# Performance work log

Hardware: AMD Instinct MI355X
Metric: run time of the kernel (lower is better)

The kernel has to match this reference:

```python
import jax, jax.numpy as jnp
import numpy as np

N = 4096        # nodes
F_IN = 256      # in_features
F_OUT = 64      # out_features
H = 64          # lstm_out_features
MAX_DEG = 64    # max neighbor count == max packed seq length
ALPHA = 0.2     # leaky relu negative slope
NEG = -9e15


def setup_inputs() -> dict:
    key = jax.random.key(0)
    ks = jax.random.split(key, 8)
    h = jax.random.normal(ks[0], (N, F_IN), dtype=jnp.float32)
    # per-node neighbor counts in [1, MAX_DEG]
    seq_length = jax.random.randint(ks[1], (N,), 1, MAX_DEG + 1, dtype=jnp.int32)
    # adjacency with exactly seq_length[i] ones in row i
    r = jax.random.uniform(ks[2], (N, N))
    ranks = jnp.argsort(jnp.argsort(-r, axis=1), axis=1)
    adj = (ranks < seq_length[:, None]).astype(jnp.float32)
    # parameters (xavier-ish scale)
    W = jax.random.normal(ks[3], (F_IN, F_OUT), dtype=jnp.float32) * (2.0 / (F_IN + F_OUT)) ** 0.5
    a = jax.random.normal(ks[4], (2 * F_OUT, 1), dtype=jnp.float32) * 0.1
    # backward-direction LSTM weights (torch gate order i,f,g,o); forward dir is unused in output
    w_ih = jax.random.normal(ks[5], (4 * H, F_OUT), dtype=jnp.float32) * 0.1
    w_hh = jax.random.normal(ks[6], (4 * H, H), dtype=jnp.float32) * 0.1
    b_ih = jnp.zeros((4 * H,), dtype=jnp.float32)
    b_hh = jnp.zeros((4 * H,), dtype=jnp.float32)
    return {"h": h, "adj": adj, "seq_length": seq_length, "W": W, "a": a,
            "w_ih": w_ih, "w_hh": w_hh, "b_ih": b_ih, "b_hh": b_hh}


def reference(h, adj, seq_length, W, a, w_ih, w_hh, b_ih, b_hh):
    n = h.shape[0]
    Wh = h @ W                                   # [N, F_OUT]
    # e[i,j] = leakyrelu(a_left . Wh_i + a_right . Wh_j)  (same math as O(N^2) concat)
    a1, a2 = a[:F_OUT, 0], a[F_OUT:, 0]
    e = jax.nn.leaky_relu((Wh @ a1)[:, None] + (Wh @ a2)[None, :], negative_slope=ALPHA)
    att = jax.nn.softmax(jnp.where(adj > 0, e, NEG), axis=1)   # [N, N]
    Wh2 = att @ Wh                               # aggregated node features [N, F_OUT]
    # sort neighbors by descending attention; LSTM only reads the first seq_length[i] <= MAX_DEG
    order = jnp.argsort(-att, axis=1)[:, :MAX_DEG]            # [N, T]
    seq = Wh2[order]                              # [N, T, F_OUT]
    # backward LSTM direction == run forward over the length-reversed sequence
    t = jnp.arange(MAX_DEG)
    rev_idx = jnp.clip(seq_length[:, None] - 1 - t[None, :], 0)
    rev = jnp.take_along_axis(seq, rev_idx[:, :, None], axis=1)  # [N, T, F_OUT]
    mask = t[None, :] < seq_length[:, None]                       # [N, T]

    def cell(carry, xm):
        hs, cs = carry
        x, m = xm                                 # x: [N, F_OUT], m: [N]
        gates = x @ w_ih.T + hs @ w_hh.T + b_ih + b_hh
        i, f, g, o = jnp.split(gates, 4, axis=1)
        c_new = jax.nn.sigmoid(f) * cs + jax.nn.sigmoid(i) * jnp.tanh(g)
        h_new = jax.nn.sigmoid(o) * jnp.tanh(c_new)
        m = m[:, None]
        return (jnp.where(m, h_new, hs), jnp.where(m, c_new, cs)), None

    init = (jnp.zeros((n, H), Wh.dtype), jnp.zeros((n, H), Wh.dtype))
    xs = (jnp.swapaxes(rev, 0, 1), mask.T)        # time-major
    (hn, _), _ = jax.lax.scan(cell, init, xs)
    return hn                                     # [N, H]  == torch hn[-1] (backward dir)
```

## Files before the change

kernel.cpp:

```cpp
#include <hip/hip_runtime.h>
#include <hip/hip_bf16.h>
#include <math.h>

#define N_NODES 4096
#define F_INN   256
#define F_OUTT  64
#define HID     64
#define MAXDEG  64

typedef __attribute__((ext_vector_type(8))) short bf16x8;
typedef __attribute__((ext_vector_type(4))) float f32x4;

__device__ int    g_mode;
__device__ int    g_anyArr[64];
__device__ float  g_Wh [N_NODES * F_OUTT];
__device__ float  g_s1 [N_NODES];
__device__ float  g_s2 [N_NODES];
__device__ int    g_rev[N_NODES * MAXDEG];
__device__ int    g_perm[N_NODES];
__device__ int    g_nbr[N_NODES * MAXDEG];
__device__ int    g_cnt[N_NODES];
__device__ float  g_WihT[64 * 256];
__device__ float  g_bias[256];
__device__ float4 g_GX [N_NODES * F_OUTT];

__device__ __forceinline__ float bf2f(unsigned short u) {
  union { unsigned int i; float f; } v; v.i = ((unsigned int)u) << 16; return v.f;
}
__device__ __forceinline__ unsigned short f2bf(float f) {
  union { __hip_bfloat16 b; unsigned short u; } v; v.b = __float2bfloat16(f); return v.u;
}

__device__ __forceinline__ float bcastf(float v, int l) {
  return __int_as_float(__builtin_amdgcn_readlane(__float_as_int(v), l));
}

__device__ __forceinline__ float rcp_fast(float x) { return __builtin_amdgcn_rcpf(x); }

__device__ __forceinline__ float sigm(float x) {
  return rcp_fast(1.f + __expf(-x));
}
__device__ __forceinline__ float tanh_fast(float x) {
  return fmaf(-2.f, rcp_fast(1.f + __expf(2.f * x)), 1.f);
}

__device__ __forceinline__ int mbcnt64(unsigned long long m) {
  return __builtin_amdgcn_mbcnt_hi((unsigned)(m >> 32),
         __builtin_amdgcn_mbcnt_lo((unsigned)(m & 0xFFFFFFFFull), 0));
}

__device__ __forceinline__ bf16x8 zfrag() {
  bf16x8 z;
  #pragma unroll
  for (int i = 0; i < 8; i++) z[i] = 0;
  return z;
}

__device__ __forceinline__ void block_sync_lds() {
  __asm__ volatile("s_waitcnt lgkmcnt(0)" ::: "memory");
  __builtin_amdgcn_s_barrier();
}

#define MFMA16(a, b, c) __builtin_amdgcn_mfma_f32_16x16x32_bf16((a), (b), (c), 0, 0, 0)

__global__ __launch_bounds__(256) void k_detect(const unsigned int* __restrict__ aw) {
  __shared__ int any;
  if (threadIdx.x == 0) any = 0;
  __syncthreads();
  const uint4 v = ((const uint4*)aw)[blockIdx.x * 256 + threadIdx.x];
  int loc = (int)((v.x & 0xFFFFu) | (v.y & 0xFFFFu) | (v.z & 0xFFFFu) | (v.w & 0xFFFFu));
  if (loc) atomicOr(&any, 1);
  __syncthreads();
  if (threadIdx.x == 0) g_anyArr[blockIdx.x] = any;
}

__global__ __launch_bounds__(256) void k_sort(const int* __restrict__ seq) {
  __shared__ int hist[MAXDEG + 1];
  __shared__ int offs[MAXDEG + 1];
  const int tid = threadIdx.x;
  if (tid <= MAXDEG) hist[tid] = 0;
  __syncthreads();
  if (tid == 0) {
    int any = 0;
    for (int b = 0; b < 64; b++) any |= g_anyArr[b];
    g_mode = any ? 1 : 0;
  }
  for (int i = tid; i < N_NODES; i += 256)
    atomicAdd(&hist[min(max(seq[i], 0), MAXDEG)], 1);
  __syncthreads();
  if (tid == 0) {
    int run = 0;
    for (int L = MAXDEG; L >= 0; L--) { offs[L] = run; run += hist[L]; }
  }
  __syncthreads();
  for (int i = tid; i < N_NODES; i += 256) {
    int p = atomicAdd(&offs[min(max(seq[i], 0), MAXDEG)], 1);
    g_perm[p] = i;
  }
}

__global__ __launch_bounds__(256) void k_scan(
    const void* __restrict__ adj, const void* __restrict__ w_ih,
    const void* __restrict__ b_ih, const void* __restrict__ b_hh)
{
  const bool bf16 = (g_mode == 1);
  const int i = blockIdx.x;
  const int w = threadIdx.x >> 6, lane = threadIdx.x & 63;
  __shared__ int seg[4][MAXDEG];
  __shared__ int scnt[4];

  if (i < 64) {
    const int unit = threadIdx.x >> 2, g = threadIdx.x & 3;
    const int src = (g * 64 + unit) * F_OUTT + i;
    g_WihT[i * 256 + threadIdx.x] =
        bf16 ? bf2f(((const unsigned short*)w_ih)[src]) : ((const float*)w_ih)[src];
  } else if (i == 64) {
    const int t = threadIdx.x;
    g_bias[t] = bf16 ? (bf2f(((const unsigned short*)b_ih)[t]) +
                        bf2f(((const unsigned short*)b_hh)[t]))
                     : (((const float*)b_ih)[t] + ((const float*)b_hh)[t]);
  }

  int base = 0;
  if (bf16) {
    const uint4* ar = (const uint4*)((const unsigned short*)adj + (size_t)i * N_NODES);
    #pragma unroll
    for (int it = 0; it < 2; it++) {
      const uint4 v = ar[w * 128 + it * 64 + lane];
      unsigned word[4] = {v.x, v.y, v.z, v.w};
      bool nz[8];
      #pragma unroll
      for (int k = 0; k < 4; k++) {
        nz[2 * k]     = (word[k] & 0x0000FFFFu) != 0u;
        nz[2 * k + 1] = (word[k] & 0xFFFF0000u) != 0u;
      }
      int pre = 0, tot = 0;
      #pragma unroll
      for (int k = 0; k < 8; k++) {
        unsigned long long bl = __ballot(nz[k]);
        pre += mbcnt64(bl);
        tot += __popcll(bl);
      }
      int loc = 0;
      #pragma unroll
      for (int k = 0; k < 8; k++) {
        if (nz[k]) {
          int p = base + pre + loc;
          if (p < MAXDEG) seg[w][p] = w * 1024 + it * 512 + lane * 8 + k;
          loc++;
        }
      }
      base += tot;
    }
  } else {
    const float4* ar = (const float4*)((const float*)adj + (size_t)i * N_NODES);
    #pragma unroll
    for (int it = 0; it < 4; it++) {
      const float4 v = ar[w * 256 + it * 64 + lane];
      bool nz[4] = {v.x != 0.0f, v.y != 0.0f, v.z != 0.0f, v.w != 0.0f};
      int pre = 0, tot = 0;
      #pragma unroll
      for (int k = 0; k < 4; k++) {
        unsigned long long bl = __ballot(nz[k]);
        pre += mbcnt64(bl);
        tot += __popcll(bl);
      }
      int loc = 0;
      #pragma unroll
      for (int k = 0; k < 4; k++) {
        if (nz[k]) {
          int p = base + pre + loc;
          if (p < MAXDEG) seg[w][p] = w * 1024 + it * 256 + lane * 4 + k;
          loc++;
        }
      }
      base += tot;
    }
  }
  if (lane == 0) scnt[w] = base;
  __syncthreads();
  int off = 0;
  #pragma unroll
  for (int u = 0; u < 4; u++) off += (u < w) ? scnt[u] : 0;
  const int cw = min(scnt[w], MAXDEG);
  if (lane < cw) {
    const int p = off + lane;
    if (p < MAXDEG) g_nbr[i * MAXDEG + p] = seg[w][lane];
  }
  if (threadIdx.x == 0)
    g_cnt[i] = min(scnt[0] + scnt[1] + scnt[2] + scnt[3], MAXDEG);
}

__global__ __launch_bounds__(256) void k_wh(
    const void* __restrict__ h, const void* __restrict__ W, const void* __restrict__ a)
{
  const bool bf16 = (g_mode == 1);
  __shared__ float Ws[F_INN * F_OUTT];
  const int tid = threadIdx.x;
  if (bf16) {
    const ushort4* Wu = (const ushort4*)W;
    for (int v = tid; v < F_INN * F_OUTT / 4; v += 256) {
      ushort4 u = Wu[v];
      ((float4*)Ws)[v] = make_float4(bf2f(u.x), bf2f(u.y), bf2f(u.z), bf2f(u.w));
    }
  } else {
    const float4* Wf = (const float4*)W;
    for (int v = tid; v < F_INN * F_OUTT / 4; v += 256) ((float4*)Ws)[v] = Wf[v];
  }
  __syncthreads();
  const int wave = tid >> 6, lane = tid & 63;
  const int row0 = blockIdx.x * 16 + wave * 4;

  float hr[4][4];
  #pragma unroll
  for (int r = 0; r < 4; r++) {
    if (bf16) {
      ushort4 v = ((const ushort4*)((const unsigned short*)h + (row0 + r) * F_INN))[lane];
      hr[0][r] = bf2f(v.x); hr[1][r] = bf2f(v.y); hr[2][r] = bf2f(v.z); hr[3][r] = bf2f(v.w);
    } else {
      float4 v = ((const float4*)((const float*)h + (row0 + r) * F_INN))[lane];
      hr[0][r] = v.x; hr[1][r] = v.y; hr[2][r] = v.z; hr[3][r] = v.w;
    }
  }

  double acc[4] = {0.0, 0.0, 0.0, 0.0};
  #pragma unroll 4
  for (int l = 0; l < 64; l++) {
    #pragma unroll
    for (int j = 0; j < 4; j++) {
      const double wd = (double)Ws[(l * 4 + j) * F_OUTT + lane];
      #pragma unroll
      for (int r = 0; r < 4; r++)
        acc[r] += (double)bcastf(hr[j][r], l) * wd;
    }
  }

  float a1, a2;
  if (bf16) {
    a1 = bf2f(((const unsigned short*)a)[lane]);
    a2 = bf2f(((const unsigned short*)a)[F_OUTT + lane]);
  } else {
    a1 = ((const float*)a)[lane];
    a2 = ((const float*)a)[F_OUTT + lane];
  }

  #pragma unroll
  for (int r = 0; r < 4; r++) {
    const float whv = (float)acc[r];
    g_Wh[(row0 + r) * F_OUTT + lane] = whv;
    double t1 = (double)whv * (double)a1;
    double t2 = (double)whv * (double)a2;
    #pragma unroll
    for (int off = 32; off > 0; off >>= 1) {
      t1 += __shfl_down(t1, off);
      t2 += __shfl_down(t2, off);
    }
    if (lane == 0) { g_s1[row0 + r] = (float)t1; g_s2[row0 + r] = (float)t2; }
  }
}

__global__ __launch_bounds__(64) void k_att2(void) {
  const int lane = threadIdx.x & 63;
  const int i = blockIdx.x;

  __shared__ int srt[MAXDEG];

  const int L = __builtin_amdgcn_readfirstlane(min(g_cnt[i], MAXDEG));
  int jn = 0;
  if (lane < L) jn = g_nbr[i * MAXDEG + lane] & (N_NODES - 1);

  const float s2v = g_s2[jn];
  float av;
  {
    float s = g_s1[i] + s2v;
    float e = (s > 0.0f) ? s : 0.2f * s;
    if (lane >= L) e = -3.0e38f;
    float m = e;
    #pragma unroll
    for (int off = 32; off > 0; off >>= 1) m = fmaxf(m, __shfl_xor(m, off));
    float p = (lane < L) ? __expf(e - m) : 0.0f;
    float ssum = p;
    #pragma unroll
    for (int off = 32; off > 0; off >>= 1) ssum += __shfl_xor(ssum, off);
    av = p * rcp_fast(ssum);
    int rank = 0;
    for (int qq = 0; qq < L; qq++) {
      const float aq = bcastf(av, qq);
      const int   jq = __builtin_amdgcn_readlane(jn, qq);
      rank += (aq > av || (aq == av && jq < jn)) ? 1 : 0;
    }
    if (lane < L) srt[rank] = jn;
  }
  g_rev[i * MAXDEG + lane] = (lane < L) ? srt[L - 1 - lane] : 0;

  float a0 = 0.f, a1 = 0.f, a2 = 0.f, a3 = 0.f;
  float a4 = 0.f, a5 = 0.f, a6 = 0.f, a7 = 0.f;
  int q = 0;
  for (; q + 8 <= L; q += 8) {
    a0 = fmaf(bcastf(av, q    ), g_Wh[(size_t)__builtin_amdgcn_readlane(jn, q    ) * F_OUTT + lane], a0);
    a1 = fmaf(bcastf(av, q + 1), g_Wh[(size_t)__builtin_amdgcn_readlane(jn, q + 1) * F_OUTT + lane], a1);
    a2 = fmaf(bcastf(av, q + 2), g_Wh[(size_t)__builtin_amdgcn_readlane(jn, q + 2) * F_OUTT + lane], a2);
    a3 = fmaf(bcastf(av, q + 3), g_Wh[(size_t)__builtin_amdgcn_readlane(jn, q + 3) * F_OUTT + lane], a3);
    a4 = fmaf(bcastf(av, q + 4), g_Wh[(size_t)__builtin_amdgcn_readlane(jn, q + 4) * F_OUTT + lane], a4);
    a5 = fmaf(bcastf(av, q + 5), g_Wh[(size_t)__builtin_amdgcn_readlane(jn, q + 5) * F_OUTT + lane], a5);
    a6 = fmaf(bcastf(av, q + 6), g_Wh[(size_t)__builtin_amdgcn_readlane(jn, q + 6) * F_OUTT + lane], a6);
    a7 = fmaf(bcastf(av, q + 7), g_Wh[(size_t)__builtin_amdgcn_readlane(jn, q + 7) * F_OUTT + lane], a7);
  }
  for (; q < L; q++)
    a0 = fmaf(bcastf(av, q), g_Wh[(size_t)__builtin_amdgcn_readlane(jn, q) * F_OUTT + lane], a0);
  const float wh2v = ((a0 + a1) + (a2 + a3)) + ((a4 + a5) + (a6 + a7));

  float gx0 = 0.f, gx1 = 0.f, gx2 = 0.f, gx3 = 0.f;
  #pragma unroll
  for (int f = 0; f < 64; f++) {
    const float wf = bcastf(wh2v, f);
    const float4 cv = *(const float4*)(g_WihT + f * 256 + lane * 4);
    gx0 = fmaf(cv.x, wf, gx0);
    gx1 = fmaf(cv.y, wf, gx1);
    gx2 = fmaf(cv.z, wf, gx2);
    gx3 = fmaf(cv.w, wf, gx3);
  }
  gx0 += g_bias[0 * 64 + lane];
  gx1 += g_bias[1 * 64 + lane];
  gx2 += g_bias[2 * 64 + lane];
  gx3 += g_bias[3 * 64 + lane];
  g_GX[(size_t)i * F_OUTT + lane] = make_float4(gx0, gx1, gx2, gx3);
}

__global__ __launch_bounds__(256, 2) void k_lstm_mfma(
    const void* __restrict__ w_hh, const int* __restrict__ seq,
    void* __restrict__ out)
{
  const bool bf16 = (g_mode == 1);
  __shared__ __align__(16) unsigned short lds_h[2][16 * 72];
  __shared__ int lds_idx[8][MAXDEG];
  const int tid = threadIdx.x;
  const int w = tid >> 6, lane = tid & 63;
  const int q = lane >> 4, c = lane & 15;
  const int rb = blockIdx.x * 8;

  for (int v = tid; v < 2 * 16 * 72; v += 256) ((unsigned short*)lds_h)[v] = 0;

  for (int v = tid; v < 8 * MAXDEG; v += 256) {
    const int e = v >> 6, t0 = v & (MAXDEG - 1);
    const int row = g_perm[rb + e] & (N_NODES - 1);
    lds_idx[e][t0] = g_rev[row * MAXDEG + t0] & (N_NODES - 1);
  }

  const int Lmax = min(max(seq[g_perm[rb] & (N_NODES - 1)], 0), MAXDEG);

  int rows_c[4];
  #pragma unroll
  for (int r = 0; r < 4; r++) rows_c[r] = min(q * 4 + r, 7);

  int row_own[2], Ls_own[2];
  #pragma unroll
  for (int k = 0; k < 2; k++) {
    row_own[k] = g_perm[rb + 2 * q + k] & (N_NODES - 1);
    Ls_own[k]  = min(max(seq[row_own[k]], 0), MAXDEG);
  }
  const int d_unit = 16 * w + c;
  const int sl = ((lane >> 5) << 4) | c;
  const bool qodd = (q & 1) != 0;

  bf16x8 Bhi[4][2];
  #pragma unroll
  for (int g = 0; g < 4; g++) {
    const int col = 64 * g + d_unit;
    #pragma unroll
    for (int ch = 0; ch < 2; ch++) {
      if (bf16) {
        Bhi[g][ch] = *(const bf16x8*)((const unsigned short*)w_hh + (size_t)col * 64 + ch * 32 + q * 8);
      } else {
        const float* wp = (const float*)w_hh + (size_t)col * 64 + ch * 32 + q * 8;
        float4 va = *(const float4*)wp, vb = *(const float4*)(wp + 4);
        bf16x8 f;
        f[0] = (short)f2bf(va.x); f[1] = (short)f2bf(va.y);
        f[2] = (short)f2bf(va.z); f[3] = (short)f2bf(va.w);
        f[4] = (short)f2bf(vb.x); f[5] = (short)f2bf(vb.y);
        f[6] = (short)f2bf(vb.z); f[7] = (short)f2bf(vb.w);
        Bhi[g][ch] = f;
      }
    }
  }

  __syncthreads();

  float4 gxb[4][4];
  #pragma unroll
  for (int s = 0; s < 4; s++) {
    #pragma unroll
    for (int r = 0; r < 4; r++)
      gxb[s][r] = g_GX[lds_idx[rows_c[r]][s] * F_OUTT + d_unit];
  }
  int idx_cur[4];
  #pragma unroll
  for (int r = 0; r < 4; r++) idx_cur[r] = lds_idx[rows_c[r]][4];

  bf16x8 h0 = zfrag(), h1 = zfrag();
  float cst[2] = {0.f, 0.f}, hst[2] = {0.f, 0.f};
  const int Lr = (Lmax + 3) & ~3;

  for (int t = 0; t < Lr; t += 4) {
    #pragma unroll
    for (int j = 0; j < 4; j++) {
      const int tt = t + j;
      f32x4 acc[4];
      #pragma unroll
      for (int g = 0; g < 4; g++) {
        f32x4 a;
        a[0] = (g==0)?gxb[j][0].x:(g==1)?gxb[j][0].y:(g==2)?gxb[j][0].z:gxb[j][0].w;
        a[1] = (g==0)?gxb[j][1].x:(g==1)?gxb[j][1].y:(g==2)?gxb[j][1].z:gxb[j][1].w;
        a[2] = (g==0)?gxb[j][2].x:(g==1)?gxb[j][2].y:(g==2)?gxb[j][2].z:gxb[j][2].w;
        a[3] = (g==0)?gxb[j][3].x:(g==1)?gxb[j][3].y:(g==2)?gxb[j][3].z:gxb[j][3].w;
        a = MFMA16(h0, Bhi[g][0], a);
        a = MFMA16(h1, Bhi[g][1], a);
        acc[g] = a;
      }
      #pragma unroll
      for (int r = 0; r < 4; r++)
        gxb[j][r] = g_GX[idx_cur[r] * F_OUTT + d_unit];
      {
        const int nt = min(tt + 5, MAXDEG - 1);
        #pragma unroll
        for (int r = 0; r < 4; r++) idx_cur[r] = lds_idx[rows_c[r]][nt];
      }
      float gv[4][2];
      #pragma unroll
      for (int g = 0; g < 4; g++) {
        float t0v = __shfl(acc[g][0], sl);
        float t1v = __shfl(acc[g][1], sl);
        float t2v = __shfl(acc[g][2], sl);
        float t3v = __shfl(acc[g][3], sl);
        gv[g][0] = qodd ? t2v : t0v;
        gv[g][1] = qodd ? t3v : t1v;
      }
      unsigned short* lh = lds_h[j & 1];
      #pragma unroll
      for (int k = 0; k < 2; k++) {
        float ig = sigm(gv[0][k]);
        float fg = sigm(gv[1][k]);
        float gg = tanh_fast(gv[2][k]);
        float og = sigm(gv[3][k]);
        float cn = fg * cst[k] + ig * gg;
        float hn = og * tanh_fast(cn);
        bool live = (tt < Ls_own[k]);
        cst[k] = live ? cn : cst[k];
        hst[k] = live ? hn : hst[k];
        lh[(2 * q + k) * 72 + d_unit] = f2bf(hst[k]);
      }
      block_sync_lds();
      {
        const unsigned short* lr_ = lds_h[j & 1] + c * 72;
        h0 = *(const bf16x8*)(lr_ + 8 * q);
        h1 = *(const bf16x8*)(lr_ + 32 + 8 * q);
      }
    }
  }
  #pragma unroll
  for (int k = 0; k < 2; k++) {
    if (bf16) ((__hip_bfloat16*)out)[row_own[k] * HID + d_unit] = __float2bfloat16(hst[k]);
    else      ((float*)out)[row_own[k] * HID + d_unit] = hst[k];
  }
}

extern "C" void kernel_launch(void* const* d_in, const int* in_sizes, int n_in,
                              void* d_out, int out_size, void* d_ws, size_t ws_size,
                              hipStream_t stream) {
  (void)in_sizes; (void)n_in; (void)out_size; (void)d_ws; (void)ws_size;
  const void* h    = d_in[0];
  const void* adj  = d_in[1];
  const int*  seq  = (const int*)d_in[2];
  const void* W    = d_in[3];
  const void* a    = d_in[4];
  const void* w_ih = d_in[5];
  const void* w_hh = d_in[6];
  const void* b_ih = d_in[7];
  const void* b_hh = d_in[8];

  k_detect   <<<64,           256, 0, stream>>>((const unsigned int*)adj);
  k_sort     <<<1,            256, 0, stream>>>(seq);
  k_scan     <<<N_NODES,      256, 0, stream>>>(adj, w_ih, b_ih, b_hh);
  k_wh       <<<N_NODES / 16, 256, 0, stream>>>(h, W, a);
  k_att2     <<<N_NODES,      64,  0, stream>>>();
  k_lstm_mfma<<<N_NODES / 8,  256, 0, stream>>>(w_hh, seq, d_out);
}
```

Before: 200.0 us.

## Run LSTM recurrence in a single wavefront per block to drop barriers

Restructures the LSTM kernel from 4 wavefronts handling 8 rows to one 64-lane wavefront handling 4 rows, so each wave computes all 16 gate column tiles with MFMA and exchanges gate values through LDS instead of shuffles. This removes the per-timestep block barrier and double-buffered hidden state, since a single wave needs no cross-wave sync. In exchange each wave issues 4x more MFMAs per step (only 4 of 16 rows useful), holds all W_hh fragments in registers, and relies on implicit wave-level ordering of LDS writes/reads without explicit waits.

Result: slower. 235.9 us (+18.0%).

```diff
diff --git a/kernel.cpp b/kernel.cpp
--- a/kernel.cpp
+++ b/kernel.cpp
@@ -56,11 +56,6 @@
   return z;
 }
 
-__device__ __forceinline__ void block_sync_lds() {
-  __asm__ volatile("s_waitcnt lgkmcnt(0)" ::: "memory");
-  __builtin_amdgcn_s_barrier();
-}
-
 #define MFMA16(a, b, c) __builtin_amdgcn_mfma_f32_16x16x32_bf16((a), (b), (c), 0, 0, 0)
 
 __global__ __launch_bounds__(256) void k_detect(const unsigned int* __restrict__ aw) {
@@ -327,140 +322,122 @@
   g_GX[(size_t)i * F_OUTT + lane] = make_float4(gx0, gx1, gx2, gx3);
 }
 
-__global__ __launch_bounds__(256, 2) void k_lstm_mfma(
+__global__ __launch_bounds__(64, 1) void k_lstm_mfma(
     const void* __restrict__ w_hh, const int* __restrict__ seq,
     void* __restrict__ out)
 {
   const bool bf16 = (g_mode == 1);
-  __shared__ __align__(16) unsigned short lds_h[2][16 * 72];
-  __shared__ int lds_idx[8][MAXDEG];
-  const int tid = threadIdx.x;
-  const int w = tid >> 6, lane = tid & 63;
+  __shared__ __align__(16) unsigned short lds_h[16 * 72];
+  __shared__ __align__(16) float lds_g[16 * 16 * 4];
+  __shared__ int lds_idx[4][MAXDEG];
+  const int lane = threadIdx.x & 63;
   const int q = lane >> 4, c = lane & 15;
-  const int rb = blockIdx.x * 8;
-
-  for (int v = tid; v < 2 * 16 * 72; v += 256) ((unsigned short*)lds_h)[v] = 0;
-
-  for (int v = tid; v < 8 * MAXDEG; v += 256) {
+  const int rb = blockIdx.x * 4;
+
+  for (int v = lane; v < 16 * 72; v += 64) lds_h[v] = 0;
+
+  for (int v = lane; v < 4 * MAXDEG; v += 64) {
     const int e = v >> 6, t0 = v & (MAXDEG - 1);
     const int row = g_perm[rb + e] & (N_NODES - 1);
     lds_idx[e][t0] = g_rev[row * MAXDEG + t0] & (N_NODES - 1);
   }
 
-  const int Lmax = min(max(seq[g_perm[rb] & (N_NODES - 1)], 0), MAXDEG);
-
-  int rows_c[4];
-  #pragma unroll
-  for (int r = 0; r < 4; r++) rows_c[r] = min(q * 4 + r, 7);
-
-  int row_own[2], Ls_own[2];
-  #pragma unroll
-  for (int k = 0; k < 2; k++) {
-    row_own[k] = g_perm[rb + 2 * q + k] & (N_NODES - 1);
-    Ls_own[k]  = min(max(seq[row_own[k]], 0), MAXDEG);
-  }
-  const int d_unit = 16 * w + c;
-  const int sl = ((lane >> 5) << 4) | c;
-  const bool qodd = (q & 1) != 0;
-
-  bf16x8 Bhi[4][2];
-  #pragma unroll
-  for (int g = 0; g < 4; g++) {
-    const int col = 64 * g + d_unit;
+  int row_own[4], Ls_own[4];
+  #pragma unroll
+  for (int r = 0; r < 4; r++) {
+    row_own[r] = g_perm[rb + r] & (N_NODES - 1);
+    Ls_own[r]  = min(max(seq[row_own[r]], 0), MAXDEG);
+  }
+  const int Lmax = max(max(Ls_own[0], Ls_own[1]), max(Ls_own[2], Ls_own[3]));
+
+  bf16x8 B[16][2];
+  #pragma unroll
+  for (int n = 0; n < 16; n++) {
     #pragma unroll
     for (int ch = 0; ch < 2; ch++) {
       if (bf16) {
-        Bhi[g][ch] = *(const bf16x8*)((const unsigned short*)w_hh + (size_t)col * 64 + ch * 32 + q * 8);
+        B[n][ch] = *(const bf16x8*)((const unsigned short*)w_hh +
+                                    (size_t)(16 * n + c) * 64 + ch * 32 + q * 8);
       } else {
-        const float* wp = (const float*)w_hh + (size_t)col * 64 + ch * 32 + q * 8;
+        const float* wp = (const float*)w_hh + (size_t)(16 * n + c) * 64 + ch * 32 + q * 8;
         float4 va = *(const float4*)wp, vb = *(const float4*)(wp + 4);
         bf16x8 f;
         f[0] = (short)f2bf(va.x); f[1] = (short)f2bf(va.y);
         f[2] = (short)f2bf(va.z); f[3] = (short)f2bf(va.w);
         f[4] = (short)f2bf(vb.x); f[5] = (short)f2bf(vb.y);
         f[6] = (short)f2bf(vb.z); f[7] = (short)f2bf(vb.w);
-        Bhi[g][ch] = f;
-      }
-    }
-  }
-
-  __syncthreads();
+        B[n][ch] = f;
+      }
+    }
+  }
 
   float4 gxb[4][4];
   #pragma unroll
   for (int s = 0; s < 4; s++) {
     #pragma unroll
     for (int r = 0; r < 4; r++)
-      gxb[s][r] = g_GX[lds_idx[rows_c[r]][s] * F_OUTT + d_unit];
+      gxb[s][r] = g_GX[lds_idx[r][s] * F_OUTT + lane];
   }
   int idx_cur[4];
   #pragma unroll
-  for (int r = 0; r < 4; r++) idx_cur[r] = lds_idx[rows_c[r]][4];
+  for (int r = 0; r < 4; r++) idx_cur[r] = lds_idx[r][4];
+
+  f32x4 zc;
+  zc[0] = 0.f; zc[1] = 0.f; zc[2] = 0.f; zc[3] = 0.f;
 
   bf16x8 h0 = zfrag(), h1 = zfrag();
-  float cst[2] = {0.f, 0.f}, hst[2] = {0.f, 0.f};
+  float cst[4] = {0.f, 0.f, 0.f, 0.f}, hst[4] = {0.f, 0.f, 0.f, 0.f};
   const int Lr = (Lmax + 3) & ~3;
 
   for (int t = 0; t < Lr; t += 4) {
     #pragma unroll
     for (int j = 0; j < 4; j++) {
       const int tt = t + j;
-      f32x4 acc[4];
-      #pragma unroll
-      for (int g = 0; g < 4; g++) {
-        f32x4 a;
-        a[0] = (g==0)?gxb[j][0].x:(g==1)?gxb[j][0].y:(g==2)?gxb[j][0].z:gxb[j][0].w;
-        a[1] = (g==0)?gxb[j][1].x:(g==1)?gxb[j][1].y:(g==2)?gxb[j][1].z:gxb[j][1].w;
-        a[2] = (g==0)?gxb[j][2].x:(g==1)?gxb[j][2].y:(g==2)?gxb[j][2].z:gxb[j][2].w;
-        a[3] = (g==0)?gxb[j][3].x:(g==1)?gxb[j][3].y:(g==2)?gxb[j][3].z:gxb[j][3].w;
-        a = MFMA16(h0, Bhi[g][0], a);
-        a = MFMA16(h1, Bhi[g][1], a);
-        acc[g] = a;
-      }
+      #pragma unroll
+      for (int n = 0; n < 16; n++) {
+        f32x4 a = MFMA16(h0, B[n][0], zc);
+        a = MFMA16(h1, B[n][1], a);
+        if (q == 0) *((f32x4*)(lds_g + (n * 16 + c) * 4)) = a;
+      }
+      float4 gxt[4];
+      #pragma unroll
+      for (int r = 0; r < 4; r++) gxt[r] = gxb[j][r];
       #pragma unroll
       for (int r = 0; r < 4; r++)
-        gxb[j][r] = g_GX[idx_cur[r] * F_OUTT + d_unit];
+        gxb[j][r] = g_GX[idx_cur[r] * F_OUTT + lane];
       {
         const int nt = min(tt + 5, MAXDEG - 1);
         #pragma unroll
-        for (int r = 0; r < 4; r++) idx_cur[r] = lds_idx[rows_c[r]][nt];
-      }
-      float gv[4][2];
-      #pragma unroll
-      for (int g = 0; g < 4; g++) {
-        float t0v = __shfl(acc[g][0], sl);
-        float t1v = __shfl(acc[g][1], sl);
-        float t2v = __shfl(acc[g][2], sl);
-        float t3v = __shfl(acc[g][3], sl);
-        gv[g][0] = qodd ? t2v : t0v;
-        gv[g][1] = qodd ? t3v : t1v;
-      }
-      unsigned short* lh = lds_h[j & 1];
-      #pragma unroll
-      for (int k = 0; k < 2; k++) {
-        float ig = sigm(gv[0][k]);
-        float fg = sigm(gv[1][k]);
-        float gg = tanh_fast(gv[2][k]);
-        float og = sigm(gv[3][k]);
-        float cn = fg * cst[k] + ig * gg;
+        for (int r = 0; r < 4; r++) idx_cur[r] = lds_idx[r][nt];
+      }
+      f32x4 gv[4];
+      #pragma unroll
+      for (int g = 0; g < 4; g++)
+        gv[g] = *((const f32x4*)(lds_g + ((g * 4 + q) * 16 + c) * 4));
+      #pragma unroll
+      for (int r = 0; r < 4; r++) {
+        float ig = sigm(gv[0][r] + gxt[r].x);
+        float fg = sigm(gv[1][r] + gxt[r].y);
+        float gg = tanh_fast(gv[2][r] + gxt[r].z);
+        float og = sigm(gv[3][r] + gxt[r].w);
+        float cn = fg * cst[r] + ig * gg;
         float hn = og * tanh_fast(cn);
-        bool live = (tt < Ls_own[k]);
-        cst[k] = live ? cn : cst[k];
-        hst[k] = live ? hn : hst[k];
-        lh[(2 * q + k) * 72 + d_unit] = f2bf(hst[k]);
-      }
-      block_sync_lds();
+        bool live = (tt < Ls_own[r]);
+        cst[r] = live ? cn : cst[r];
+        hst[r] = live ? hn : hst[r];
+        lds_h[r * 72 + lane] = f2bf(hst[r]);
+      }
       {
-        const unsigned short* lr_ = lds_h[j & 1] + c * 72;
+        const unsigned short* lr_ = lds_h + c * 72;
         h0 = *(const bf16x8*)(lr_ + 8 * q);
         h1 = *(const bf16x8*)(lr_ + 32 + 8 * q);
       }
     }
   }
   #pragma unroll
-  for (int k = 0; k < 2; k++) {
-    if (bf16) ((__hip_bfloat16*)out)[row_own[k] * HID + d_unit] = __float2bfloat16(hst[k]);
-    else      ((float*)out)[row_own[k] * HID + d_unit] = hst[k];
+  for (int r = 0; r < 4; r++) {
+    if (bf16) ((__hip_bfloat16*)out)[row_own[r] * HID + lane] = __float2bfloat16(hst[r]);
+    else      ((float*)out)[row_own[r] * HID + lane] = hst[r];
   }
 }
 
@@ -483,5 +460,5 @@
   k_scan     <<<N_NODES,      256, 0, stream>>>(adj, w_ih, b_ih, b_hh);
   k_wh       <<<N_NODES / 16, 256, 0, stream>>>(h, W, a);
   k_att2     <<<N_NODES,      64,  0, stream>>>();
-  k_lstm_mfma<<<N_NODES / 8,  256, 0, stream>>>(w_hh, seq, d_out);
-}
+  k_lstm_mfma<<<N_NODES / 4,  64,  0, stream>>>(w_hh, seq, d_out);
+}
```
